# Kernel tuning notes

Measured on AMD Instinct MI355X. Metric: run time of the kernel, lower is better.

The kernel has to match this reference:

```python
import jax, jax.numpy as jnp
import numpy as np

NUM_SEGMENTS = 64  # batch_size, = batch_indices.max()+1 by construction


def setup_inputs() -> dict:
    key = jax.random.key(0)
    k1, k2 = jax.random.split(key)
    N, D = 1048576, 256
    features = jax.random.normal(k1, (N, D), dtype=jnp.float32)
    batch_indices = jnp.sort(jax.random.randint(k2, (N,), 0, NUM_SEGMENTS, dtype=jnp.int64))
    return {"features": features, "batch_indices": batch_indices}


def reference(features, batch_indices):
    # features: [N, D], batch_indices: [N] -> out: [B, 2*D]
    idx = batch_indices.astype(jnp.int32)
    counts = jax.ops.segment_sum(jnp.ones_like(features[:, 0]), idx,
                                 num_segments=NUM_SEGMENTS)  # [B]
    sums = jax.ops.segment_sum(features, idx, num_segments=NUM_SEGMENTS)  # [B, D]
    nonempty = counts > 0
    mean_feat = sums / jnp.maximum(counts, 1.0)[:, None]
    maxs = jax.ops.segment_max(features, idx, num_segments=NUM_SEGMENTS)  # [B, D]
    max_feat = jnp.where(nonempty[:, None], maxs, 0.0)
    mean_feat = jnp.where(nonempty[:, None], mean_feat, 0.0)
    return jnp.concatenate([mean_feat, max_feat], axis=1)  # [B, 2*D]
```

## Files before the change

kernel.cpp:

```cpp
#include <hip/hip_runtime.h>
#include <math.h>

#define D 256
#define SEGS 64
#define RPB 512
#define THREADS 256

typedef float f32x4 __attribute__((ext_vector_type(4)));

__device__ __forceinline__ unsigned enc_f32(float f) {
  unsigned u = __float_as_uint(f);
  return (u & 0x80000000u) ? ~u : (u | 0x80000000u);
}
__device__ __forceinline__ float dec_f32(unsigned k) {
  unsigned u = (k & 0x80000000u) ? (k ^ 0x80000000u) : ~k;
  return __uint_as_float(u);
}

__global__ void init_kernel(const int* __restrict__ idx, int n,
                            float* __restrict__ sums,
                            unsigned* __restrict__ maxk,
                            int* __restrict__ bounds) {
  const int s = blockIdx.x;
  if (threadIdx.x < D) {
    sums[s * D + threadIdx.x] = 0.0f;
    maxk[s * D + threadIdx.x] = 0u;
  }
  if (threadIdx.x == 0) {
    const int stride = (idx[(size_t)n - 1] == 0) ? 2 : 1;
    const int v = s + 1;
    int lo = 0, hi = n;
    while (lo < hi) {
      int mid = (lo + hi) >> 1;
      if (idx[(size_t)mid * stride] < v) lo = mid + 1; else hi = mid;
    }
    bounds[s + 1] = lo;
    if (s == 0) bounds[0] = 0;
  }
}

__global__ __launch_bounds__(THREADS, 4)
void agg_kernel(const float* __restrict__ feat, const int* __restrict__ bounds,
                float* __restrict__ sums, unsigned* __restrict__ maxk, int n) {
  const int lane = threadIdx.x & 63;
  const int wave = threadIdx.x >> 6;
  int i = blockIdx.x * RPB + wave * (RPB / 4);
  const int re = min(i + (RPB / 4), n);
  if (i >= re) return;

  const int b_end = bounds[lane + 1];
  int cur = (int)__popcll(__ballot(b_end <= i));

  const float* base = feat + lane * 4;

  while (true) {
    const int e = __shfl(b_end, cur);
    const int j = min(re, e);

    f32x4 sum = {0.f, 0.f, 0.f, 0.f};
    f32x4 mx  = {-INFINITY, -INFINITY, -INFINITY, -INFINITY};
#pragma unroll 8
    for (int k = i; k < j; ++k) {
      const f32x4 v = __builtin_nontemporal_load(
          reinterpret_cast<const f32x4*>(base + (size_t)k * D));
      sum += v;
      mx.x = __builtin_fmaxf(mx.x, v.x);
      mx.y = __builtin_fmaxf(mx.y, v.y);
      mx.z = __builtin_fmaxf(mx.z, v.z);
      mx.w = __builtin_fmaxf(mx.w, v.w);
    }

    float* sp = sums + cur * D + lane * 4;
    atomicAdd(sp + 0, sum.x); atomicAdd(sp + 1, sum.y);
    atomicAdd(sp + 2, sum.z); atomicAdd(sp + 3, sum.w);
    unsigned* mp = maxk + cur * D + lane * 4;
    atomicMax(mp + 0, enc_f32(mx.x)); atomicMax(mp + 1, enc_f32(mx.y));
    atomicMax(mp + 2, enc_f32(mx.z)); atomicMax(mp + 3, enc_f32(mx.w));

    if (j >= re) break;
    i = j;
    do { ++cur; } while (__shfl(b_end, cur) <= i);
  }
}

__global__ void finalize_kernel(const float* __restrict__ sums,
                                const unsigned* __restrict__ maxk,
                                const int* __restrict__ bounds,
                                float* __restrict__ out) {
  int t = blockIdx.x * blockDim.x + threadIdx.x;
  if (t >= SEGS * 2 * D) return;
  int s = t / (2 * D);
  int j = t % (2 * D);
  int c = bounds[s + 1] - bounds[s];
  float v;
  if (j < D)
    v = (c > 0) ? sums[s * D + j] / (float)c : 0.0f;
  else
    v = (c > 0) ? dec_f32(maxk[s * D + (j - D)]) : 0.0f;
  out[t] = v;
}

extern "C" void kernel_launch(void* const* d_in, const int* in_sizes, int n_in,
                              void* d_out, int out_size, void* d_ws, size_t ws_size,
                              hipStream_t stream) {
  const float* feat = (const float*)d_in[0];
  const int*   idx  = (const int*)d_in[1];
  const int n = in_sizes[1];
  float* out = (float*)d_out;

  char* ws = (char*)d_ws;
  float*    sums   = (float*)ws;
  unsigned* maxk   = (unsigned*)(ws + SEGS * D * 4);
  int*      bounds = (int*)(ws + 2 * SEGS * D * 4);

  init_kernel<<<SEGS, THREADS, 0, stream>>>(idx, n, sums, maxk, bounds);

  const int nblocks = (n + RPB - 1) / RPB;
  agg_kernel<<<nblocks, THREADS, 0, stream>>>(feat, bounds, sums, maxk, n);

  finalize_kernel<<<(SEGS * 2 * D + THREADS - 1) / THREADS, THREADS, 0, stream>>>(
      sums, maxk, bounds, out);
}
```

Measured before the change: 217.8 us.

## Reduce atomics with block-level LDS reduction and parallel boundary search

Rows per block grow fourfold, and blocks whose rows all fall in one segment combine the four waves' partial sum and max in LDS before a single set of atomics per column. This cuts global atomic traffic. The init kernel now finds segment bounds with a parallel scan over all rows, detecting where the index changes, instead of 64 serial binary searches. Occupancy hint drops to 2 blocks per CU, and the grid has fewer, longer-running blocks, which may hurt load balance and latency hiding.

```diff
diff --git a/kernel.cpp b/kernel.cpp
--- a/kernel.cpp
+++ b/kernel.cpp
@@ -3,8 +3,9 @@
 
 #define D 256
 #define SEGS 64
-#define RPB 512
+#define RPB 2048
 #define THREADS 256
+#define RPW (RPB / 4)
 
 typedef float f32x4 __attribute__((ext_vector_type(4)));
 
@@ -21,38 +22,66 @@
                             float* __restrict__ sums,
                             unsigned* __restrict__ maxk,
                             int* __restrict__ bounds) {
-  const int s = blockIdx.x;
-  if (threadIdx.x < D) {
-    sums[s * D + threadIdx.x] = 0.0f;
-    maxk[s * D + threadIdx.x] = 0u;
-  }
-  if (threadIdx.x == 0) {
-    const int stride = (idx[(size_t)n - 1] == 0) ? 2 : 1;
-    const int v = s + 1;
-    int lo = 0, hi = n;
-    while (lo < hi) {
-      int mid = (lo + hi) >> 1;
-      if (idx[(size_t)mid * stride] < v) lo = mid + 1; else hi = mid;
-    }
-    bounds[s + 1] = lo;
-    if (s == 0) bounds[0] = 0;
+  const int gid = blockIdx.x * blockDim.x + threadIdx.x;
+  if (gid < SEGS * D) { sums[gid] = 0.0f; maxk[gid] = 0u; }
+  const int stride = (idx[(size_t)n - 1] == 0) ? 2 : 1;
+  const int gsz = gridDim.x * blockDim.x;
+  for (int i = gid; i <= n; i += gsz) {
+    const int prev = (i == 0) ? -1 : idx[(size_t)(i - 1) * stride];
+    const int curv = (i == n) ? SEGS : idx[(size_t)i * stride];
+    for (int s = prev + 1; s <= curv; ++s) bounds[s] = i;
   }
 }
 
-__global__ __launch_bounds__(THREADS, 4)
+__global__ __launch_bounds__(THREADS, 2)
 void agg_kernel(const float* __restrict__ feat, const int* __restrict__ bounds,
                 float* __restrict__ sums, unsigned* __restrict__ maxk, int n) {
+  __shared__ f32x4 lds_s[4][64];
+  __shared__ f32x4 lds_m[4][64];
+
   const int lane = threadIdx.x & 63;
   const int wave = threadIdx.x >> 6;
-  int i = blockIdx.x * RPB + wave * (RPB / 4);
-  const int re = min(i + (RPB / 4), n);
-  if (i >= re) return;
+  const int r0 = blockIdx.x * RPB;
+  const int rows = min(RPB, n - r0);
 
   const int b_end = bounds[lane + 1];
-  int cur = (int)__popcll(__ballot(b_end <= i));
+  const int segF = (int)__popcll(__ballot(b_end <= r0));
+  const int segL = (int)__popcll(__ballot(b_end <= r0 + rows - 1));
 
+  int i = r0 + wave * RPW;
+  const int re = min(i + RPW, n);
   const float* base = feat + lane * 4;
 
+  if (segF == segL) {
+    f32x4 sum = {0.f, 0.f, 0.f, 0.f};
+    f32x4 mx  = {-INFINITY, -INFINITY, -INFINITY, -INFINITY};
+#pragma unroll 8
+    for (int k = i; k < re; ++k) {
+      const f32x4 v = __builtin_nontemporal_load(
+          reinterpret_cast<const f32x4*>(base + (size_t)k * D));
+      sum += v;
+      mx.x = __builtin_fmaxf(mx.x, v.x);
+      mx.y = __builtin_fmaxf(mx.y, v.y);
+      mx.z = __builtin_fmaxf(mx.z, v.z);
+      mx.w = __builtin_fmaxf(mx.w, v.w);
+    }
+    lds_s[wave][lane] = sum;
+    lds_m[wave][lane] = mx;
+    __syncthreads();
+    const int c = threadIdx.x;
+    float s = 0.0f, m = -INFINITY;
+#pragma unroll
+    for (int w = 0; w < 4; ++w) {
+      s += ((const float*)&lds_s[w][c >> 2])[c & 3];
+      m = __builtin_fmaxf(m, ((const float*)&lds_m[w][c >> 2])[c & 3]);
+    }
+    atomicAdd(&sums[segF * D + c], s);
+    atomicMax(&maxk[segF * D + c], enc_f32(m));
+    return;
+  }
+
+  if (i >= re) return;
+  int cur = (int)__popcll(__ballot(b_end <= i));
   while (true) {
     const int e = __shfl(b_end, cur);
     const int j = min(re, e);
@@ -113,7 +142,7 @@
   unsigned* maxk   = (unsigned*)(ws + SEGS * D * 4);
   int*      bounds = (int*)(ws + 2 * SEGS * D * 4);
 
-  init_kernel<<<SEGS, THREADS, 0, stream>>>(idx, n, sums, maxk, bounds);
+  init_kernel<<<1024, THREADS, 0, stream>>>(idx, n, sums, maxk, bounds);
 
   const int nblocks = (n + RPB - 1) / RPB;
   agg_kernel<<<nblocks, THREADS, 0, stream>>>(feat, bounds, sums, maxk, n);
```

New measurement: 264.9 us. 1.22x slower.
